# Kernel tuning notes

Hardware: AMD Instinct MI355X
Metric: run time of the kernel (lower is better)

Reference implementation:

```python
import jax, jax.numpy as jnp
import numpy as np
from jax import lax

EPS = 1e-5
DN = ('NCHW', 'OIHW', 'NCHW')

def ternarize(w):
    # TWN-style ternarization: delta = 0.7*mean|w|, alpha = mean of |w| above threshold
    a = jnp.abs(w)
    delta = 0.7 * jnp.mean(a)
    mask = (a > delta).astype(w.dtype)
    alpha = jnp.sum(a * mask) / jnp.maximum(jnp.sum(mask), 1.0)
    return alpha * jnp.sign(w) * mask

def conv(x, w, stride=1, pad=0, groups=1):
    return lax.conv_general_dilated(
        x, w, (stride, stride), [(pad, pad), (pad, pad)],
        feature_group_count=groups, dimension_numbers=DN)

def batchnorm(x, gamma, beta):
    # training-mode BN: per-channel batch statistics over (N,H,W)
    mean = jnp.mean(x, axis=(0, 2, 3), keepdims=True)
    var = jnp.var(x, axis=(0, 2, 3), keepdims=True)
    inv = lax.rsqrt(var + EPS)
    return (x - mean) * inv * gamma[None, :, None, None] + beta[None, :, None, None]

def setup_inputs() -> dict:
    key = jax.random.key(0)
    ks = jax.random.split(key, 10)
    B, Cin, H, W = 32, 96, 56, 56
    planes, Cout = 576, 96
    return {
        'x':  jax.random.normal(ks[0], (B, Cin, H, W), jnp.float32),
        'w1': jax.random.normal(ks[1], (planes, Cin, 1, 1), jnp.float32) * 0.1,
        'g1': jax.random.uniform(ks[2], (planes,), jnp.float32, 0.5, 1.5),
        'b1': jax.random.normal(ks[3], (planes,), jnp.float32) * 0.1,
        'w2': jax.random.normal(ks[4], (planes, 1, 3, 3), jnp.float32) * 0.1,
        'g2': jax.random.uniform(ks[5], (planes,), jnp.float32, 0.5, 1.5),
        'b2': jax.random.normal(ks[6], (planes,), jnp.float32) * 0.1,
        'w3': jax.random.normal(ks[7], (Cout, planes, 1, 1), jnp.float32) * 0.1,
        'g3': jax.random.uniform(ks[8], (Cout,), jnp.float32, 0.5, 1.5),
        'b3': jax.random.normal(ks[9], (Cout,), jnp.float32) * 0.1,
    }

def reference(x, w1, g1, b1, w2, g2, b2, w3, g3, b3):
    planes = w1.shape[0]
    # expand 1x1 (ternary) + BN + ReLU
    out = jax.nn.relu(batchnorm(conv(x, ternarize(w1)), g1, b1))
    # depthwise 3x3 stride 1 (ternary) + BN + ReLU
    out = jax.nn.relu(batchnorm(conv(out, ternarize(w2), stride=1, pad=1, groups=planes), g2, b2))
    # project 1x1 (ternary) + BN
    out = batchnorm(conv(out, ternarize(w3)), g3, b3)
    # stride==1 and in_planes==out_planes -> identity shortcut
    return out + x
```

## Files before the change

kernel.cpp:

```cpp
#include <hip/hip_runtime.h>
#include <hip/hip_bf16.h>

#define BATCH 32
#define CIN 96
#define HW 3136
#define PL 576
#define COUT 96
#define NT 49
#define NHW 100352.0

typedef __attribute__((ext_vector_type(4))) float f32x4;
typedef __attribute__((ext_vector_type(8))) short s16x8;

__device__ __forceinline__ unsigned short f2b(float v) {
  __hip_bfloat16 h = __float2bfloat16(v);
  return *reinterpret_cast<unsigned short*>(&h);
}
__device__ __forceinline__ float b2f(unsigned int u) {
  return __uint_as_float((u & 0xffffu) << 16);
}

__global__ __launch_bounds__(256) void absred_kernel(const float* __restrict__ w,
                                                     float* __restrict__ part, int n4) {
  __shared__ float ra[256];
  const int tid = threadIdx.x;
  float s = 0.f;
  for (int i = blockIdx.x * 256 + tid; i < n4; i += 32 * 256) {
    float4 v = reinterpret_cast<const float4*>(w)[i];
    s += fabsf(v.x) + fabsf(v.y) + fabsf(v.z) + fabsf(v.w);
  }
  ra[tid] = s; __syncthreads();
  for (int off = 128; off; off >>= 1) { if (tid < off) ra[tid] += ra[tid + off]; __syncthreads(); }
  if (tid == 0) part[blockIdx.x] = ra[0];
}

__device__ __forceinline__ float delta_from_parts(const float* __restrict__ part, float invn) {
  float s = 0.f;
#pragma unroll
  for (int i = 0; i < 32; ++i) s += part[i];
  return 0.7f * s * invn;
}

__global__ __launch_bounds__(256) void ternw_bf16_kernel(
    const float* __restrict__ w, const float* __restrict__ part, float invn,
    __hip_bfloat16* __restrict__ tw, int n4) {
  const float delta = delta_from_parts(part, invn);
  const int i = blockIdx.x * 256 + threadIdx.x;
  if (i >= n4) return;
  float4 v = reinterpret_cast<const float4*>(w)[i];
  float vv[4] = {v.x, v.y, v.z, v.w};
  unsigned short b[4];
#pragma unroll
  for (int j = 0; j < 4; ++j)
    b[j] = (fabsf(vv[j]) > delta)
               ? (unsigned short)(0x3F80u | ((__float_as_uint(vv[j]) >> 16) & 0x8000u))
               : (unsigned short)0;
  unsigned lo = (unsigned)b[0] | ((unsigned)b[1] << 16);
  unsigned hi = (unsigned)b[2] | ((unsigned)b[3] << 16);
  reinterpret_cast<uint2*>(tw)[i] = make_uint2(lo, hi);
}

__global__ __launch_bounds__(256) void ternw_f32_kernel(
    const float* __restrict__ w, const float* __restrict__ part, float invn,
    float* __restrict__ tw, int n4) {
  const float delta = delta_from_parts(part, invn);
  const int i = blockIdx.x * 256 + threadIdx.x;
  if (i >= n4) return;
  float4 v = reinterpret_cast<const float4*>(w)[i];
  float4 o;
  o.x = (fabsf(v.x) > delta) ? (v.x > 0.f ? 1.f : -1.f) : 0.f;
  o.y = (fabsf(v.y) > delta) ? (v.y > 0.f ? 1.f : -1.f) : 0.f;
  o.z = (fabsf(v.z) > delta) ? (v.z > 0.f ? 1.f : -1.f) : 0.f;
  o.w = (fabsf(v.w) > delta) ? (v.w > 0.f ? 1.f : -1.f) : 0.f;
  reinterpret_cast<float4*>(tw)[i] = o;
}

__global__ __launch_bounds__(256) void bnp_kernel(
    const float* __restrict__ psum, const float* __restrict__ psumsq,
    const float* __restrict__ gamma, const float* __restrict__ beta,
    float* __restrict__ sc, float* __restrict__ sh, int nparts) {
  const int ch = blockIdx.x, tid = threadIdx.x;
  double s = 0.0, q = 0.0;
  for (int i = tid; i < nparts; i += 256) {
    s += (double)psum[(size_t)ch * nparts + i];
    q += (double)psumsq[(size_t)ch * nparts + i];
  }
  __shared__ double rs[256], rq[256];
  rs[tid] = s; rq[tid] = q; __syncthreads();
  for (int off = 128; off; off >>= 1) {
    if (tid < off) { rs[tid] += rs[tid + off]; rq[tid] += rq[tid + off]; }
    __syncthreads();
  }
  if (tid == 0) {
    double mean = rs[0] / NHW;
    double var = rq[0] / NHW - mean * mean;
    float inv = (float)(1.0 / sqrt(var + 1e-5));
    float g = gamma[ch];
    sc[ch] = inv * g;
    sh[ch] = beta[ch] - (float)mean * inv * g;
  }
}

__global__ __launch_bounds__(256) void conv1_mfma(
    const float* __restrict__ x, const __hip_bfloat16* __restrict__ tw1,
    __hip_bfloat16* __restrict__ o1c,
    float* __restrict__ psum, float* __restrict__ psumsq) {
  __shared__ __hip_bfloat16 Bt[64 * 104];
  const int hwt = blockIdx.x, n = blockIdx.y, mt = blockIdx.z;
  const int t0 = hwt * 64;
  const int tid = threadIdx.x;
  const int lane = tid & 63, w = tid >> 6;

  {
    const float* xp = x + (size_t)n * CIN * HW + t0 + lane;
    const int cb = w * 24;
#pragma unroll
    for (int i6 = 0; i6 < 6; ++i6) {
      const int c0 = cb + i6 * 4;
      float v0 = xp[(size_t)(c0 + 0) * HW];
      float v1 = xp[(size_t)(c0 + 1) * HW];
      float v2 = xp[(size_t)(c0 + 2) * HW];
      float v3 = xp[(size_t)(c0 + 3) * HW];
      unsigned lo = (unsigned)f2b(v0) | ((unsigned)f2b(v1) << 16);
      unsigned hi = (unsigned)f2b(v2) | ((unsigned)f2b(v3) << 16);
      *reinterpret_cast<uint2*>(&Bt[lane * 104 + c0]) = make_uint2(lo, hi);
    }
  }
  __syncthreads();

  const int l15 = lane & 15, lh = lane >> 4;
  f32x4 acc[3][4];
#pragma unroll
  for (int f = 0; f < 3; ++f)
#pragma unroll
    for (int g = 0; g < 4; ++g) acc[f][g] = (f32x4){0.f, 0.f, 0.f, 0.f};
  const int rowb = mt * 192 + w * 48;
#pragma unroll
  for (int k0 = 0; k0 < 3; ++k0) {
    s16x8 a[3], b[4];
#pragma unroll
    for (int f = 0; f < 3; ++f)
      a[f] = *reinterpret_cast<const s16x8*>(tw1 + (size_t)(rowb + f * 16 + l15) * CIN + k0 * 32 + lh * 8);
#pragma unroll
    for (int g = 0; g < 4; ++g)
      b[g] = *reinterpret_cast<const s16x8*>(&Bt[(g * 16 + l15) * 104 + k0 * 32 + lh * 8]);
#pragma unroll
    for (int f = 0; f < 3; ++f)
#pragma unroll
      for (int g = 0; g < 4; ++g)
        acc[f][g] = __builtin_amdgcn_mfma_f32_16x16x32_bf16(a[f], b[g], acc[f][g], 0, 0, 0);
  }

#pragma unroll
  for (int f = 0; f < 3; ++f) {
    float sred[4] = {0.f, 0.f, 0.f, 0.f};
    float qred[4] = {0.f, 0.f, 0.f, 0.f};
    const int ch0 = rowb + f * 16 + lh * 4;
#pragma unroll
    for (int g = 0; g < 4; ++g) {
      unsigned p0 = (unsigned)f2b(acc[f][g][0]) | ((unsigned)f2b(acc[f][g][1]) << 16);
      unsigned p1 = (unsigned)f2b(acc[f][g][2]) | ((unsigned)f2b(acc[f][g][3]) << 16);
      const int hw = t0 + g * 16 + l15;
      *reinterpret_cast<uint2*>(o1c + ((size_t)n * HW + hw) * PL + ch0) = make_uint2(p0, p1);
#pragma unroll
      for (int r = 0; r < 4; ++r) {
        float v = acc[f][g][r];
        sred[r] += v; qred[r] = fmaf(v, v, qred[r]);
      }
    }
#pragma unroll
    for (int r = 0; r < 4; ++r) {
      float s = sred[r], q = qred[r];
#pragma unroll
      for (int m = 1; m < 16; m <<= 1) { s += __shfl_xor(s, m); q += __shfl_xor(q, m); }
      if (l15 == 0) {
        const int pi = (ch0 + r) * 1568 + n * NT + hwt;
        psum[pi] = s; psumsq[pi] = q;
      }
    }
  }
}

__global__ __launch_bounds__(64) void dw_kernel(
    const __hip_bfloat16* __restrict__ o1c, const float* __restrict__ tw2,
    const float* __restrict__ s1, const float* __restrict__ t1,
    __hip_bfloat16* __restrict__ o2c,
    float* __restrict__ psum, float* __restrict__ psumsq) {
  const int strip = blockIdx.x, kh = blockIdx.y, n = blockIdx.z;
  const int lane = threadIdx.x;
  const int col = lane >> 3, chs = lane & 7;
  const int c = strip * 8 + col;
  const int chb = kh * 32 + chs * 4;
  const int ec = (col == 0) ? (c - 1) : (c + 1);
  const bool eok = (col == 0) ? (c > 0) : ((col == 7) ? (c < 55) : false);

  float sc[4], sh[4], wt[9][4];
#pragma unroll
  for (int j = 0; j < 4; ++j) {
    sc[j] = s1[chb + j]; sh[j] = t1[chb + j];
#pragma unroll
    for (int t = 0; t < 9; ++t) wt[t][j] = tw2[(chb + j) * 9 + t];
  }

  const size_t nb = (size_t)n * HW;
  const __hip_bfloat16* pc = o1c + (nb + c) * PL + chb;
  const __hip_bfloat16* pe = o1c + (nb + ((eok ? ec : c))) * PL + chb;
  __hip_bfloat16* po = o2c + (nb + c) * PL + chb;

  float Al[4], Ac[4], Ar[4], Bl[4], Bc[4], Br[4], Cl[4], Cc[4], Cr[4];
  float psc[4] = {0.f, 0.f, 0.f, 0.f}, psq[4] = {0.f, 0.f, 0.f, 0.f};

#define ROWW(Rl, Rc, Rr, q_) do {                                              \
    const int q__ = (q_);                                                      \
    uint2 rc_ = make_uint2(0u, 0u), re_ = make_uint2(0u, 0u);                  \
    if (q__ < 56) {                                                            \
      rc_ = *reinterpret_cast<const uint2*>(pc + (size_t)q__ * 56 * PL);       \
      if (eok) re_ = *reinterpret_cast<const uint2*>(pe + (size_t)q__ * 56 * PL); \
    }                                                                          \
    float cen[4], ee[4];                                                       \
    cen[0] = fmaxf(fmaf(b2f(rc_.x), sc[0], sh[0]), 0.f);                       \
    cen[1] = fmaxf(fmaf(b2f(rc_.x >> 16), sc[1], sh[1]), 0.f);                 \
    cen[2] = fmaxf(fmaf(b2f(rc_.y), sc[2], sh[2]), 0.f);                       \
    cen[3] = fmaxf(fmaf(b2f(rc_.y >> 16), sc[3], sh[3]), 0.f);                 \
    ee[0] = fmaxf(fmaf(b2f(re_.x), sc[0], sh[0]), 0.f);                        \
    ee[1] = fmaxf(fmaf(b2f(re_.x >> 16), sc[1], sh[1]), 0.f);                  \
    ee[2] = fmaxf(fmaf(b2f(re_.y), sc[2], sh[2]), 0.f);                        \
    ee[3] = fmaxf(fmaf(b2f(re_.y >> 16), sc[3], sh[3]), 0.f);                  \
    if (q__ >= 56) { cen[0]=cen[1]=cen[2]=cen[3]=0.f; }                        \
    if (q__ >= 56 || !eok) { ee[0]=ee[1]=ee[2]=ee[3]=0.f; }                    \
    _Pragma("unroll")                                                          \
    for (int j = 0; j < 4; ++j) {                                              \
      float lv = __shfl(cen[j], lane - 8);                                     \
      float rv = __shfl(cen[j], lane + 8);                                     \
      Rc[j] = cen[j];                                                          \
      Rl[j] = (col == 0) ? ee[j] : lv;                                         \
      Rr[j] = (col == 7) ? ee[j] : rv;                                         \
    }                                                                          \
  } while (0)

#define STEP(M1l, M1c, M1r, R0l, R0c, R0r, P1l, P1c, P1r, q_) do {             \
    ROWW(P1l, P1c, P1r, (q_) + 1);                                             \
    unsigned pk0, pk1;                                                         \
    {                                                                          \
      float o_[4];                                                             \
      _Pragma("unroll")                                                        \
      for (int j = 0; j < 4; ++j) {                                            \
        float a_ = wt[0][j] * M1l[j];                                          \
        a_ = fmaf(wt[1][j], M1c[j], a_);                                       \
        a_ = fmaf(wt[2][j], M1r[j], a_);                                       \
        a_ = fmaf(wt[3][j], R0l[j], a_);                                       \
        a_ = fmaf(wt[4][j], R0c[j], a_);                                       \
        a_ = fmaf(wt[5][j], R0r[j], a_);                                       \
        a_ = fmaf(wt[6][j], P1l[j], a_);                                       \
        a_ = fmaf(wt[7][j], P1c[j], a_);                                       \
        a_ = fmaf(wt[8][j], P1r[j], a_);                                       \
        o_[j] = a_;                                                            \
        psc[j] += a_; psq[j] = fmaf(a_, a_, psq[j]);                           \
      }                                                                        \
      pk0 = (unsigned)f2b(o_[0]) | ((unsigned)f2b(o_[1]) << 16);               \
      pk1 = (unsigned)f2b(o_[2]) | ((unsigned)f2b(o_[3]) << 16);               \
    }                                                                          \
    *reinterpret_cast<uint2*>(po + (size_t)(q_) * 56 * PL) = make_uint2(pk0, pk1); \
  } while (0)

#pragma unroll
  for (int j = 0; j < 4; ++j) { Al[j] = 0.f; Ac[j] = 0.f; Ar[j] = 0.f; }
  ROWW(Bl, Bc, Br, 0);
  for (int t = 0; t < 18; ++t) {
    STEP(Al, Ac, Ar, Bl, Bc, Br, Cl, Cc, Cr, 3 * t);
    STEP(Bl, Bc, Br, Cl, Cc, Cr, Al, Ac, Ar, 3 * t + 1);
    STEP(Cl, Cc, Cr, Al, Ac, Ar, Bl, Bc, Br, 3 * t + 2);
  }
  STEP(Al, Ac, Ar, Bl, Bc, Br, Cl, Cc, Cr, 54);
  STEP(Bl, Bc, Br, Cl, Cc, Cr, Al, Ac, Ar, 55);
#undef STEP
#undef ROWW

#pragma unroll
  for (int m = 8; m <= 32; m <<= 1)
#pragma unroll
    for (int j = 0; j < 4; ++j) { psc[j] += __shfl_xor(psc[j], m); psq[j] += __shfl_xor(psq[j], m); }
  if (col == 0) {
#pragma unroll
    for (int j = 0; j < 4; ++j) {
      const int pi = (chb + j) * 224 + n * 7 + strip;
      psum[pi] = psc[j]; psumsq[pi] = psq[j];
    }
  }
}

__global__ __launch_bounds__(256) void conv3_mfma(
    const __hip_bfloat16* __restrict__ o2c, const __hip_bfloat16* __restrict__ tw3,
    const float* __restrict__ s2, const float* __restrict__ t2,
    __hip_bfloat16* __restrict__ out3,
    float* __restrict__ psum, float* __restrict__ psumsq) {
  __shared__ __hip_bfloat16 chunk[2][64 * 64];
  __shared__ float smem[96 * 65];
  __shared__ float s2s[PL], t2s[PL];
  const int hwt = blockIdx.x, n = blockIdx.y, tid = threadIdx.x;
  const int lane = tid & 63, w = tid >> 6;
  const int l15 = lane & 15, lh = lane >> 4;
  const int wm = w >> 1, wn = w & 1;
  const int t0 = hwt * 64;
  for (int i = tid; i < PL; i += 256) { s2s[i] = s2[i]; t2s[i] = t2[i]; }

  const int hwp = tid >> 2;
  const int cq = tid & 3;
  const __hip_bfloat16* src = o2c + ((size_t)n * HW + t0 + hwp) * PL + cq * 16;
  uint4 ra = *reinterpret_cast<const uint4*>(src);
  uint4 rb = *reinterpret_cast<const uint4*>(src + 8);

  f32x4 acc[3][2];
#pragma unroll
  for (int f = 0; f < 3; ++f)
#pragma unroll
    for (int g = 0; g < 2; ++g) acc[f][g] = (f32x4){0.f, 0.f, 0.f, 0.f};

  const unsigned key = (unsigned)((hwp & 7) << 4);
  __syncthreads();

  for (int kc = 0; kc < 9; ++kc) {
    const int cur = kc & 1;
    {
      const int cb16 = kc * 64 + cq * 16;
      unsigned uu[8] = {ra.x, ra.y, ra.z, ra.w, rb.x, rb.y, rb.z, rb.w};
      unsigned po[8];
#pragma unroll
      for (int j = 0; j < 8; ++j) {
        float lo = fmaxf(fmaf(b2f(uu[j]),       s2s[cb16 + 2 * j],     t2s[cb16 + 2 * j]), 0.f);
        float hi = fmaxf(fmaf(b2f(uu[j] >> 16), s2s[cb16 + 2 * j + 1], t2s[cb16 + 2 * j + 1]), 0.f);
        po[j] = (unsigned)f2b(lo) | ((unsigned)f2b(hi) << 16);
      }
      char* base = (char*)&chunk[cur][0] + hwp * 128;
      *reinterpret_cast<uint4*>(base + (((unsigned)(cq * 32)) ^ key)) =
          make_uint4(po[0], po[1], po[2], po[3]);
      *reinterpret_cast<uint4*>(base + (((unsigned)(cq * 32 + 16)) ^ key)) =
          make_uint4(po[4], po[5], po[6], po[7]);
    }
    __syncthreads();
    if (kc < 8) {
      ra = *reinterpret_cast<const uint4*>(src + (kc + 1) * 64);
      rb = *reinterpret_cast<const uint4*>(src + (kc + 1) * 64 + 8);
    }
#pragma unroll
    for (int kb = 0; kb < 2; ++kb) {
      s16x8 a[3];
#pragma unroll
      for (int f = 0; f < 3; ++f)
        a[f] = *reinterpret_cast<const s16x8*>(
            tw3 + (size_t)(wm * 48 + f * 16 + l15) * PL + kc * 64 + kb * 32 + lh * 8);
#pragma unroll
      for (int g = 0; g < 2; ++g) {
        const int row = wn * 32 + g * 16 + l15;
        const unsigned cbyte = (unsigned)(kb * 64 + lh * 16) ^ (unsigned)((row & 7) << 4);
        const s16x8 b = *reinterpret_cast<const s16x8*>(
            (const char*)&chunk[cur][0] + row * 128 + cbyte);
#pragma unroll
        for (int f = 0; f < 3; ++f)
          acc[f][g] = __builtin_amdgcn_mfma_f32_16x16x32_bf16(a[f], b, acc[f][g], 0, 0, 0);
      }
    }
  }
  __syncthreads();
#pragma unroll
  for (int f = 0; f < 3; ++f)
#pragma unroll
    for (int g = 0; g < 2; ++g)
#pragma unroll
      for (int r = 0; r < 4; ++r)
        smem[(wm * 48 + f * 16 + lh * 4 + r) * 65 + wn * 32 + g * 16 + l15] = acc[f][g][r];
  __syncthreads();
  const int slot = tid & 7, rgrp = tid >> 3;
#pragma unroll
  for (int s = 0; s < 3; ++s) {
    const int rl = s * 32 + rgrp;
    float v[8], sm = 0.f, sq = 0.f;
#pragma unroll
    for (int j = 0; j < 8; ++j) {
      float t = smem[rl * 65 + slot * 8 + j];
      v[j] = t; sm += t; sq = fmaf(t, t, sq);
    }
    unsigned pk[4];
#pragma unroll
    for (int j = 0; j < 4; ++j) pk[j] = (unsigned)f2b(v[2 * j]) | ((unsigned)f2b(v[2 * j + 1]) << 16);
    *reinterpret_cast<uint4*>(out3 + ((size_t)n * COUT + rl) * HW + t0 + slot * 8) =
        make_uint4(pk[0], pk[1], pk[2], pk[3]);
#pragma unroll
    for (int m = 1; m < 8; m <<= 1) { sm += __shfl_xor(sm, m, 8); sq += __shfl_xor(sq, m, 8); }
    if (slot == 0) { int pi = rl * 1568 + n * NT + hwt; psum[pi] = sm; psumsq[pi] = sq; }
  }
}

__global__ __launch_bounds__(256) void final_kernel(
    const __hip_bfloat16* __restrict__ out3, const float* __restrict__ x,
    const float* __restrict__ s3, const float* __restrict__ t3,
    float* __restrict__ out) {
  const int i = blockIdx.x * 256 + threadIdx.x;
  const int p = (i * 4) / HW;
  const int co = p - (p / COUT) * COUT;
  uint2 raw = reinterpret_cast<const uint2*>(out3)[i];
  float4 b = reinterpret_cast<const float4*>(x)[i];
  const float scv = s3[co], tv = t3[co];
  float4 r;
  r.x = fmaf(b2f(raw.x), scv, tv) + b.x;
  r.y = fmaf(b2f(raw.x >> 16), scv, tv) + b.y;
  r.z = fmaf(b2f(raw.y), scv, tv) + b.z;
  r.w = fmaf(b2f(raw.y >> 16), scv, tv) + b.w;
  reinterpret_cast<float4*>(out)[i] = r;
}

extern "C" void kernel_launch(void* const* d_in, const int* in_sizes, int n_in,
                              void* d_out, int out_size, void* d_ws, size_t ws_size,
                              hipStream_t stream) {
  const float* x  = (const float*)d_in[0];
  const float* w1 = (const float*)d_in[1];
  const float* g1 = (const float*)d_in[2];
  const float* b1 = (const float*)d_in[3];
  const float* w2 = (const float*)d_in[4];
  const float* g2 = (const float*)d_in[5];
  const float* b2 = (const float*)d_in[6];
  const float* w3 = (const float*)d_in[7];
  const float* g3 = (const float*)d_in[8];
  const float* b3 = (const float*)d_in[9];
  float* out = (float*)d_out;

  char* ws = (char*)d_ws;
  __hip_bfloat16* tw1b = (__hip_bfloat16*)(ws + 0);
  __hip_bfloat16* tw3b = (__hip_bfloat16*)(ws + 110592);
  float* tw2f = (float*)(ws + 221184);
  float* s1 = (float*)(ws + 241920);
  float* t1 = s1 + PL; float* s2 = t1 + PL; float* t2 = s2 + PL;
  float* s3 = (float*)(ws + 251136); float* t3 = s3 + COUT;
  float* ps1 = (float*)(ws + 251904);
  float* pq1 = ps1 + PL * 1568;
  float* ps2 = pq1 + PL * 1568;
  float* pq2 = ps2 + PL * 1568;
  float* ps3 = pq2 + PL * 1568;
  float* pq3 = ps3 + COUT * 1568;
  float* part1 = pq3 + COUT * 1568;
  float* part2 = part1 + 32;
  float* part3 = part2 + 32;
  __hip_bfloat16* o1c = (__hip_bfloat16*)(ws + 16777216);
  __hip_bfloat16* o2c = o1c + (size_t)BATCH * HW * PL;
  __hip_bfloat16* out3b = o1c;

  absred_kernel<<<32, 256, 0, stream>>>(w1, part1, 13824);
  absred_kernel<<<32, 256, 0, stream>>>(w2, part2, 1296);
  absred_kernel<<<32, 256, 0, stream>>>(w3, part3, 13824);
  ternw_bf16_kernel<<<54, 256, 0, stream>>>(w1, part1, 1.0f / 55296.0f, tw1b, 13824);
  ternw_f32_kernel <<<6, 256, 0, stream>>>(w2, part2, 1.0f / 5184.0f, tw2f, 1296);
  ternw_bf16_kernel<<<54, 256, 0, stream>>>(w3, part3, 1.0f / 55296.0f, tw3b, 13824);

  conv1_mfma<<<dim3(NT, BATCH, 3), 256, 0, stream>>>(x, tw1b, o1c, ps1, pq1);
  bnp_kernel<<<PL, 256, 0, stream>>>(ps1, pq1, g1, b1, s1, t1, 1568);

  dw_kernel<<<dim3(7, 18, BATCH), 64, 0, stream>>>(o1c, tw2f, s1, t1, o2c, ps2, pq2);
  bnp_kernel<<<PL, 256, 0, stream>>>(ps2, pq2, g2, b2, s2, t2, 224);

  conv3_mfma<<<dim3(NT, BATCH), 256, 0, stream>>>(o2c, tw3b, s2, t2, out3b, ps3, pq3);
  bnp_kernel<<<COUT, 256, 0, stream>>>(ps3, pq3, g3, b3, s3, t3, 1568);

  final_kernel<<<out_size / 1024, 256, 0, stream>>>(out3b, x, s3, t3, out);
}
```

Measured before the change: 280.8 us.

## Recompute expand conv in fused depthwise kernel instead of storing expanded activations

The expand 1x1 conv now runs only to collect BN statistics and no longer writes the 576-channel intermediate. A new fused kernel recomputes the expand conv per 8x8 spatial tile with a 1-pixel halo, taking input from a bf16 channels-last copy of x. It applies BN1+ReLU in shared memory and then runs the depthwise 3x3 from LDS. This removes a large bf16 intermediate write and read at the cost of computing the expand GEMM twice, plus halo overhead of about 1.56x in the fused pass.

```diff
diff --git a/kernel.cpp b/kernel.cpp
--- a/kernel.cpp
+++ b/kernel.cpp
@@ -101,16 +101,12 @@
   }
 }
 
-__global__ __launch_bounds__(256) void conv1_mfma(
-    const float* __restrict__ x, const __hip_bfloat16* __restrict__ tw1,
-    __hip_bfloat16* __restrict__ o1c,
-    float* __restrict__ psum, float* __restrict__ psumsq) {
+__global__ __launch_bounds__(256) void xcast_kernel(const float* __restrict__ x,
+                                                    __hip_bfloat16* __restrict__ xb) {
   __shared__ __hip_bfloat16 Bt[64 * 104];
-  const int hwt = blockIdx.x, n = blockIdx.y, mt = blockIdx.z;
-  const int t0 = hwt * 64;
-  const int tid = threadIdx.x;
+  const int hwt = blockIdx.x, n = blockIdx.y;
+  const int t0 = hwt * 64, tid = threadIdx.x;
   const int lane = tid & 63, w = tid >> 6;
-
   {
     const float* xp = x + (size_t)n * CIN * HW + t0 + lane;
     const int cb = w * 24;
@@ -127,7 +123,36 @@
     }
   }
   __syncthreads();
-
+  for (int i = tid; i < 768; i += 256) {
+    const int hw = i / 12, oct = i - hw * 12;
+    uint4 v = *reinterpret_cast<const uint4*>(&Bt[hw * 104 + oct * 8]);
+    *reinterpret_cast<uint4*>(xb + ((size_t)(n * HW + t0 + hw)) * 96 + oct * 8) = v;
+  }
+}
+
+__global__ __launch_bounds__(256) void conv1_stats(
+    const float* __restrict__ x, const __hip_bfloat16* __restrict__ tw1,
+    float* __restrict__ psum, float* __restrict__ psumsq) {
+  __shared__ __hip_bfloat16 Bt[64 * 104];
+  const int hwt = blockIdx.x, n = blockIdx.y, mt = blockIdx.z;
+  const int t0 = hwt * 64, tid = threadIdx.x;
+  const int lane = tid & 63, w = tid >> 6;
+  {
+    const float* xp = x + (size_t)n * CIN * HW + t0 + lane;
+    const int cb = w * 24;
+#pragma unroll
+    for (int i6 = 0; i6 < 6; ++i6) {
+      const int c0 = cb + i6 * 4;
+      float v0 = xp[(size_t)(c0 + 0) * HW];
+      float v1 = xp[(size_t)(c0 + 1) * HW];
+      float v2 = xp[(size_t)(c0 + 2) * HW];
+      float v3 = xp[(size_t)(c0 + 3) * HW];
+      unsigned lo = (unsigned)f2b(v0) | ((unsigned)f2b(v1) << 16);
+      unsigned hi = (unsigned)f2b(v2) | ((unsigned)f2b(v3) << 16);
+      *reinterpret_cast<uint2*>(&Bt[lane * 104 + c0]) = make_uint2(lo, hi);
+    }
+  }
+  __syncthreads();
   const int l15 = lane & 15, lh = lane >> 4;
   f32x4 acc[3][4];
 #pragma unroll
@@ -150,24 +175,18 @@
       for (int g = 0; g < 4; ++g)
         acc[f][g] = __builtin_amdgcn_mfma_f32_16x16x32_bf16(a[f], b[g], acc[f][g], 0, 0, 0);
   }
-
 #pragma unroll
   for (int f = 0; f < 3; ++f) {
     float sred[4] = {0.f, 0.f, 0.f, 0.f};
     float qred[4] = {0.f, 0.f, 0.f, 0.f};
     const int ch0 = rowb + f * 16 + lh * 4;
 #pragma unroll
-    for (int g = 0; g < 4; ++g) {
-      unsigned p0 = (unsigned)f2b(acc[f][g][0]) | ((unsigned)f2b(acc[f][g][1]) << 16);
-      unsigned p1 = (unsigned)f2b(acc[f][g][2]) | ((unsigned)f2b(acc[f][g][3]) << 16);
-      const int hw = t0 + g * 16 + l15;
-      *reinterpret_cast<uint2*>(o1c + ((size_t)n * HW + hw) * PL + ch0) = make_uint2(p0, p1);
+    for (int g = 0; g < 4; ++g)
 #pragma unroll
       for (int r = 0; r < 4; ++r) {
         float v = acc[f][g][r];
         sred[r] += v; qred[r] = fmaf(v, v, qred[r]);
       }
-    }
 #pragma unroll
     for (int r = 0; r < 4; ++r) {
       float s = sred[r], q = qred[r];
@@ -181,110 +200,133 @@
   }
 }
 
-__global__ __launch_bounds__(64) void dw_kernel(
-    const __hip_bfloat16* __restrict__ o1c, const float* __restrict__ tw2,
-    const float* __restrict__ s1, const float* __restrict__ t1,
-    __hip_bfloat16* __restrict__ o2c,
+__global__ __launch_bounds__(256) void fused_kernel(
+    const __hip_bfloat16* __restrict__ xb, const __hip_bfloat16* __restrict__ tw1,
+    const float* __restrict__ tw2, const float* __restrict__ s1,
+    const float* __restrict__ t1, __hip_bfloat16* __restrict__ o2c,
     float* __restrict__ psum, float* __restrict__ psumsq) {
-  const int strip = blockIdx.x, kh = blockIdx.y, n = blockIdx.z;
-  const int lane = threadIdx.x;
-  const int col = lane >> 3, chs = lane & 7;
-  const int c = strip * 8 + col;
-  const int chb = kh * 32 + chs * 4;
-  const int ec = (col == 0) ? (c - 1) : (c + 1);
-  const bool eok = (col == 0) ? (c > 0) : ((col == 7) ? (c < 55) : false);
-
-  float sc[4], sh[4], wt[9][4];
-#pragma unroll
-  for (int j = 0; j < 4; ++j) {
-    sc[j] = s1[chb + j]; sh[j] = t1[chb + j];
-#pragma unroll
-    for (int t = 0; t < 9; ++t) wt[t][j] = tw2[(chb + j) * 9 + t];
-  }
-
-  const size_t nb = (size_t)n * HW;
-  const __hip_bfloat16* pc = o1c + (nb + c) * PL + chb;
-  const __hip_bfloat16* pe = o1c + (nb + ((eok ? ec : c))) * PL + chb;
-  __hip_bfloat16* po = o2c + (nb + c) * PL + chb;
-
-  float Al[4], Ac[4], Ar[4], Bl[4], Bc[4], Br[4], Cl[4], Cc[4], Cr[4];
-  float psc[4] = {0.f, 0.f, 0.f, 0.f}, psq[4] = {0.f, 0.f, 0.f, 0.f};
-
-#define ROWW(Rl, Rc, Rr, q_) do {                                              \
-    const int q__ = (q_);                                                      \
-    uint2 rc_ = make_uint2(0u, 0u), re_ = make_uint2(0u, 0u);                  \
-    if (q__ < 56) {                                                            \
-      rc_ = *reinterpret_cast<const uint2*>(pc + (size_t)q__ * 56 * PL);       \
-      if (eok) re_ = *reinterpret_cast<const uint2*>(pe + (size_t)q__ * 56 * PL); \
-    }                                                                          \
-    float cen[4], ee[4];                                                       \
-    cen[0] = fmaxf(fmaf(b2f(rc_.x), sc[0], sh[0]), 0.f);                       \
-    cen[1] = fmaxf(fmaf(b2f(rc_.x >> 16), sc[1], sh[1]), 0.f);                 \
-    cen[2] = fmaxf(fmaf(b2f(rc_.y), sc[2], sh[2]), 0.f);                       \
-    cen[3] = fmaxf(fmaf(b2f(rc_.y >> 16), sc[3], sh[3]), 0.f);                 \
-    ee[0] = fmaxf(fmaf(b2f(re_.x), sc[0], sh[0]), 0.f);                        \
-    ee[1] = fmaxf(fmaf(b2f(re_.x >> 16), sc[1], sh[1]), 0.f);                  \
-    ee[2] = fmaxf(fmaf(b2f(re_.y), sc[2], sh[2]), 0.f);                        \
-    ee[3] = fmaxf(fmaf(b2f(re_.y >> 16), sc[3], sh[3]), 0.f);                  \
-    if (q__ >= 56) { cen[0]=cen[1]=cen[2]=cen[3]=0.f; }                        \
-    if (q__ >= 56 || !eok) { ee[0]=ee[1]=ee[2]=ee[3]=0.f; }                    \
-    _Pragma("unroll")                                                          \
-    for (int j = 0; j < 4; ++j) {                                              \
-      float lv = __shfl(cen[j], lane - 8);                                     \
-      float rv = __shfl(cen[j], lane + 8);                                     \
-      Rc[j] = cen[j];                                                          \
-      Rl[j] = (col == 0) ? ee[j] : lv;                                         \
-      Rr[j] = (col == 7) ? ee[j] : rv;                                         \
-    }                                                                          \
-  } while (0)
-
-#define STEP(M1l, M1c, M1r, R0l, R0c, R0r, P1l, P1c, P1r, q_) do {             \
-    ROWW(P1l, P1c, P1r, (q_) + 1);                                             \
-    unsigned pk0, pk1;                                                         \
-    {                                                                          \
-      float o_[4];                                                             \
-      _Pragma("unroll")                                                        \
-      for (int j = 0; j < 4; ++j) {                                            \
-        float a_ = wt[0][j] * M1l[j];                                          \
-        a_ = fmaf(wt[1][j], M1c[j], a_);                                       \
-        a_ = fmaf(wt[2][j], M1r[j], a_);                                       \
-        a_ = fmaf(wt[3][j], R0l[j], a_);                                       \
-        a_ = fmaf(wt[4][j], R0c[j], a_);                                       \
-        a_ = fmaf(wt[5][j], R0r[j], a_);                                       \
-        a_ = fmaf(wt[6][j], P1l[j], a_);                                       \
-        a_ = fmaf(wt[7][j], P1c[j], a_);                                       \
-        a_ = fmaf(wt[8][j], P1r[j], a_);                                       \
-        o_[j] = a_;                                                            \
-        psc[j] += a_; psq[j] = fmaf(a_, a_, psq[j]);                           \
-      }                                                                        \
-      pk0 = (unsigned)f2b(o_[0]) | ((unsigned)f2b(o_[1]) << 16);               \
-      pk1 = (unsigned)f2b(o_[2]) | ((unsigned)f2b(o_[3]) << 16);               \
-    }                                                                          \
-    *reinterpret_cast<uint2*>(po + (size_t)(q_) * 56 * PL) = make_uint2(pk0, pk1); \
-  } while (0)
-
-#pragma unroll
-  for (int j = 0; j < 4; ++j) { Al[j] = 0.f; Ac[j] = 0.f; Ar[j] = 0.f; }
-  ROWW(Bl, Bc, Br, 0);
-  for (int t = 0; t < 18; ++t) {
-    STEP(Al, Ac, Ar, Bl, Bc, Br, Cl, Cc, Cr, 3 * t);
-    STEP(Bl, Bc, Br, Cl, Cc, Cr, Al, Ac, Ar, 3 * t + 1);
-    STEP(Cl, Cc, Cr, Al, Ac, Ar, Bl, Bc, Br, 3 * t + 2);
-  }
-  STEP(Al, Ac, Ar, Bl, Bc, Br, Cl, Cc, Cr, 54);
-  STEP(Bl, Bc, Br, Cl, Cc, Cr, Al, Ac, Ar, 55);
-#undef STEP
-#undef ROWW
-
-#pragma unroll
-  for (int m = 8; m <= 32; m <<= 1)
-#pragma unroll
-    for (int j = 0; j < 4; ++j) { psc[j] += __shfl_xor(psc[j], m); psq[j] += __shfl_xor(psq[j], m); }
-  if (col == 0) {
+  __shared__ __hip_bfloat16 Bts[112 * 104];
+  __shared__ __hip_bfloat16 ot[100 * 76];
+  __shared__ float wsh[9 * 64];
+  __shared__ float red0[4 * 64], red1[4 * 64];
+  const int tb = blockIdx.x, n = blockIdx.y;
+  const int tr0 = (tb / 7) * 8, tc0 = (tb - (tb / 7) * 7) * 8;
+  const int tid = threadIdx.x;
+  const int lane = tid & 63, wm = tid >> 6;
+  const int l15 = lane & 15, lh = lane >> 4;
+
+  for (int i = tid; i < 1344; i += 256) {
+    const int pos = i / 12, oct = i - pos * 12;
+    uint4 v = make_uint4(0u, 0u, 0u, 0u);
+    if (pos < 100) {
+      const int hr = pos / 10, hc = pos - hr * 10;
+      const int r = tr0 + hr - 1, c = tc0 + hc - 1;
+      if ((unsigned)r < 56u && (unsigned)c < 56u)
+        v = *reinterpret_cast<const uint4*>(xb + (size_t)(n * HW + r * 56 + c) * 96 + oct * 8);
+    }
+    *reinterpret_cast<uint4*>(&Bts[pos * 104 + oct * 8]) = v;
+  }
+  __syncthreads();
+
+  const int q4 = tid & 15, pgrp = tid >> 4;
+
+  for (int kc = 0; kc < 9; ++kc) {
+    for (int i = tid; i < 576; i += 256) {
+      const int chl = i / 9, tap = i - chl * 9;
+      wsh[tap * 64 + chl] = tw2[kc * 576 + i];
+    }
+    f32x4 acc[7];
+#pragma unroll
+    for (int g = 0; g < 7; ++g) acc[g] = (f32x4){0.f, 0.f, 0.f, 0.f};
+    const int rowc = kc * 64 + wm * 16;
+#pragma unroll
+    for (int k0 = 0; k0 < 3; ++k0) {
+      const s16x8 a = *reinterpret_cast<const s16x8*>(
+          tw1 + (size_t)(rowc + l15) * CIN + k0 * 32 + lh * 8);
+#pragma unroll
+      for (int g = 0; g < 7; ++g) {
+        const s16x8 b = *reinterpret_cast<const s16x8*>(
+            &Bts[(g * 16 + l15) * 104 + k0 * 32 + lh * 8]);
+        acc[g] = __builtin_amdgcn_mfma_f32_16x16x32_bf16(a, b, acc[g], 0, 0, 0);
+      }
+    }
+    float scv[4], shv[4];
+#pragma unroll
+    for (int r = 0; r < 4; ++r) {
+      const int ch = rowc + lh * 4 + r;
+      scv[r] = s1[ch]; shv[r] = t1[ch];
+    }
+#pragma unroll
+    for (int g = 0; g < 7; ++g) {
+      const int pos = g * 16 + l15;
+      if (pos < 100) {
+        const int hr = pos / 10, hc = pos - hr * 10;
+        const int r = tr0 + hr - 1, c = tc0 + hc - 1;
+        uint2 pk = make_uint2(0u, 0u);
+        if ((unsigned)r < 56u && (unsigned)c < 56u) {
+          float v0 = fmaxf(fmaf(acc[g][0], scv[0], shv[0]), 0.f);
+          float v1 = fmaxf(fmaf(acc[g][1], scv[1], shv[1]), 0.f);
+          float v2 = fmaxf(fmaf(acc[g][2], scv[2], shv[2]), 0.f);
+          float v3 = fmaxf(fmaf(acc[g][3], scv[3], shv[3]), 0.f);
+          pk.x = (unsigned)f2b(v0) | ((unsigned)f2b(v1) << 16);
+          pk.y = (unsigned)f2b(v2) | ((unsigned)f2b(v3) << 16);
+        }
+        *reinterpret_cast<uint2*>(&ot[pos * 76 + wm * 16 + lh * 4]) = pk;
+      }
+    }
+    __syncthreads();
+
+    float wt[9][4];
+#pragma unroll
+    for (int tap = 0; tap < 9; ++tap) {
+      const f32x4 wv = *reinterpret_cast<const f32x4*>(&wsh[tap * 64 + q4 * 4]);
+      wt[tap][0] = wv[0]; wt[tap][1] = wv[1]; wt[tap][2] = wv[2]; wt[tap][3] = wv[3];
+    }
+    float psc[4] = {0.f, 0.f, 0.f, 0.f}, psq[4] = {0.f, 0.f, 0.f, 0.f};
+#pragma unroll
+    for (int u = 0; u < 4; ++u) {
+      const int opos = pgrp * 4 + u;
+      const int orr = opos >> 3, oc = opos & 7;
+      float av[4] = {0.f, 0.f, 0.f, 0.f};
+#pragma unroll
+      for (int dy = 0; dy < 3; ++dy)
+#pragma unroll
+        for (int dx = 0; dx < 3; ++dx) {
+          const int hpos = (orr + dy) * 10 + (oc + dx);
+          const uint2 rv = *reinterpret_cast<const uint2*>(&ot[hpos * 76 + q4 * 4]);
+          const int tap = dy * 3 + dx;
+          av[0] = fmaf(wt[tap][0], b2f(rv.x), av[0]);
+          av[1] = fmaf(wt[tap][1], b2f(rv.x >> 16), av[1]);
+          av[2] = fmaf(wt[tap][2], b2f(rv.y), av[2]);
+          av[3] = fmaf(wt[tap][3], b2f(rv.y >> 16), av[3]);
+        }
+      unsigned p0 = (unsigned)f2b(av[0]) | ((unsigned)f2b(av[1]) << 16);
+      unsigned p1 = (unsigned)f2b(av[2]) | ((unsigned)f2b(av[3]) << 16);
+      *reinterpret_cast<uint2*>(
+          o2c + (size_t)(n * HW + (tr0 + orr) * 56 + tc0 + oc) * PL + kc * 64 + q4 * 4) =
+          make_uint2(p0, p1);
+#pragma unroll
+      for (int j = 0; j < 4; ++j) { psc[j] += av[j]; psq[j] = fmaf(av[j], av[j], psq[j]); }
+    }
 #pragma unroll
     for (int j = 0; j < 4; ++j) {
-      const int pi = (chb + j) * 224 + n * 7 + strip;
-      psum[pi] = psc[j]; psumsq[pi] = psq[j];
+      psc[j] += __shfl_xor(psc[j], 16); psc[j] += __shfl_xor(psc[j], 32);
+      psq[j] += __shfl_xor(psq[j], 16); psq[j] += __shfl_xor(psq[j], 32);
+    }
+    if ((tid & 63) < 16) {
+      const int wv_ = tid >> 6;
+#pragma unroll
+      for (int j = 0; j < 4; ++j) {
+        red0[wv_ * 64 + q4 * 4 + j] = psc[j];
+        red1[wv_ * 64 + q4 * 4 + j] = psq[j];
+      }
+    }
+    __syncthreads();
+    if (tid < 64) {
+      float a = red0[tid] + red0[64 + tid] + red0[128 + tid] + red0[192 + tid];
+      float b = red1[tid] + red1[64 + tid] + red1[128 + tid] + red1[192 + tid];
+      const int pi = (kc * 64 + tid) * 1568 + n * NT + tb;
+      psum[pi] = a; psumsq[pi] = b;
     }
   }
 }
@@ -440,9 +482,9 @@
   float* part1 = pq3 + COUT * 1568;
   float* part2 = part1 + 32;
   float* part3 = part2 + 32;
-  __hip_bfloat16* o1c = (__hip_bfloat16*)(ws + 16777216);
-  __hip_bfloat16* o2c = o1c + (size_t)BATCH * HW * PL;
-  __hip_bfloat16* out3b = o1c;
+  __hip_bfloat16* xb    = (__hip_bfloat16*)(ws + 16777216);
+  __hip_bfloat16* o2c   = (__hip_bfloat16*)(ws + 36175872);
+  __hip_bfloat16* out3b = (__hip_bfloat16*)(ws + 151781376);
 
   absred_kernel<<<32, 256, 0, stream>>>(w1, part1, 13824);
   absred_kernel<<<32, 256, 0, stream>>>(w2, part2, 1296);
@@ -451,11 +493,12 @@
   ternw_f32_kernel <<<6, 256, 0, stream>>>(w2, part2, 1.0f / 5184.0f, tw2f, 1296);
   ternw_bf16_kernel<<<54, 256, 0, stream>>>(w3, part3, 1.0f / 55296.0f, tw3b, 13824);
 
-  conv1_mfma<<<dim3(NT, BATCH, 3), 256, 0, stream>>>(x, tw1b, o1c, ps1, pq1);
+  xcast_kernel<<<dim3(NT, BATCH), 256, 0, stream>>>(x, xb);
+  conv1_stats<<<dim3(NT, BATCH, 3), 256, 0, stream>>>(x, tw1b, ps1, pq1);
   bnp_kernel<<<PL, 256, 0, stream>>>(ps1, pq1, g1, b1, s1, t1, 1568);
 
-  dw_kernel<<<dim3(7, 18, BATCH), 64, 0, stream>>>(o1c, tw2f, s1, t1, o2c, ps2, pq2);
-  bnp_kernel<<<PL, 256, 0, stream>>>(ps2, pq2, g2, b2, s2, t2, 224);
+  fused_kernel<<<dim3(NT, BATCH), 256, 0, stream>>>(xb, tw1b, tw2f, s1, t1, o2c, ps2, pq2);
+  bnp_kernel<<<PL, 256, 0, stream>>>(ps2, pq2, g2, b2, s2, t2, 1568);
 
   conv3_mfma<<<dim3(NT, BATCH), 256, 0, stream>>>(o2c, tw3b, s2, t2, out3b, ps3, pq3);
   bnp_kernel<<<COUT, 256, 0, stream>>>(ps3, pq3, g3, b3, s3, t3, 1568);
```

New measurement: 291.6 us. 1.04x slower.
